# Kernel tuning notes

Measured on AMD Instinct MI355X. Metric: run time of the kernel, lower is better.

## Reference

```python
import jax, jax.numpy as jnp
import numpy as np

B, T, C = 4, 4096, 512
H = 64           # head_size
GRAN = 128       # staircase granularity


def staircase_mask(t, g):
    # tril OR block-diagonal blocks of size g (the staircase fills the upper
    # triangle inside each gxg diagonal block)
    i = jnp.arange(t)
    return (i[:, None] >= i[None, :]) | ((i[:, None] // g) == (i[None, :] // g))


def setup_inputs() -> dict:
    key = jax.random.key(0)
    kx, kk, kq, kv = jax.random.split(key, 4)
    scale = 0.02
    return {
        "x": jax.random.normal(kx, (B, T, C), dtype=jnp.float32),
        "Wk": jax.random.normal(kk, (C, H), dtype=jnp.float32) * scale,
        "Wq": jax.random.normal(kq, (C, H), dtype=jnp.float32) * scale,
        "Wv": jax.random.normal(kv, (C, H), dtype=jnp.float32) * scale,
    }


def reference(x, Wk, Wq, Wv):
    # single head of self-attention with staircase mask (dropout off / eval mode)
    k = x @ Wk          # [B,T,H]
    q = x @ Wq          # [B,T,H]
    v = x @ Wv          # [B,T,H]
    wei = jnp.einsum("bth,bsh->bts", q, k) * (H ** -0.5)   # [B,T,T]
    mask = staircase_mask(T, GRAN)                           # [T,T] bool
    wei = jnp.where(mask, wei, -jnp.inf)
    wei = jax.nn.softmax(wei, axis=-1)
    out = jnp.einsum("bts,bsh->bth", wei, v)                 # [B,T,H]
    return out
```

## Files before the change

kernel.cpp:

```cpp
#include <hip/hip_runtime.h>

typedef unsigned short u16;
typedef unsigned int u32;
typedef unsigned long long u64;
typedef __attribute__((ext_vector_type(8))) short short8;
typedef __attribute__((ext_vector_type(4))) float f32x4;

#define T_ 4096
#define QSCALE 0.18033688f
#define CH 2
#define SBAT 1088
#define PSTRIDE 36

#if __has_builtin(__builtin_amdgcn_exp2f)
#define EXP2F(x) __builtin_amdgcn_exp2f(x)
#else
#define EXP2F(x) exp2f(x)
#endif

__device__ __forceinline__ u16 f2bf(float f) {
    unsigned u = __float_as_uint(f);
    u += 0x7FFFu + ((u >> 16) & 1u);
    return (u16)(u >> 16);
}

__global__ __launch_bounds__(256) void wtrans_kernel(
    const float* __restrict__ Wq, const float* __restrict__ Wk,
    const float* __restrict__ Wv, u16* __restrict__ WTf)
{
    const int tid  = blockIdx.x * 256 + threadIdx.x;
    const int frag = tid >> 6;
    const int lane = tid & 63;
    const int ng   = frag >> 4;
    const int kc   = frag & 15;
    const int m    = ng >> 2;
    const float* W = (m == 0) ? Wq : (m == 1) ? Wk : Wv;
    const int h  = (ng & 3) * 16 + (lane & 15);
    const int c0 = kc * 32 + (lane >> 4) * 8;
    short8 v;
    #pragma unroll
    for (int j = 0; j < 8; ++j)
        v[j] = (short)f2bf(W[(c0 + j) * 64 + h]);
    *(short8*)(WTf + (size_t)frag * 512 + lane * 8) = v;
}

__global__ __launch_bounds__(256) void proj_kernel(
    const float* __restrict__ x, const u16* __restrict__ WTf,
    u16* __restrict__ Qf, u16* __restrict__ Kf, u16* __restrict__ Vf)
{
    __shared__ u16 xs[16 * 520];
    __shared__ u16 img[3072];
    const int t    = threadIdx.x;
    const int lane = t & 63;
    const int w    = t >> 6;
    const int l16  = lane & 15;
    const int quad = lane >> 4;
    const int rowbase = blockIdx.x * 16;
    const int bat  = rowbase >> 12;
    const int tloc = rowbase & 4095;

    #pragma unroll
    for (int it = 0; it < 8; ++it) {
        int f   = t + it * 256;
        int row = f >> 7;
        int c4  = (f & 127) * 4;
        f32x4 a = *(const f32x4*)(x + (size_t)(rowbase + row) * 512 + c4);
        unsigned lo = (unsigned)f2bf(a[0]) | ((unsigned)f2bf(a[1]) << 16);
        unsigned hi = (unsigned)f2bf(a[2]) | ((unsigned)f2bf(a[3]) << 16);
        *(uint2*)(xs + row * 520 + c4) = make_uint2(lo, hi);
    }
    __syncthreads();

    f32x4 acc[3];
    #pragma unroll
    for (int nt = 0; nt < 3; ++nt) acc[nt] = (f32x4){0.f, 0.f, 0.f, 0.f};

    const u16* ab = xs + l16 * 520 + quad * 8;
    const u16* wb = WTf + (size_t)(w * 3 * 16) * 512 + lane * 8;

    #pragma unroll 4
    for (int kc = 0; kc < 16; ++kc) {
        short8 af = *(const short8*)(ab + kc * 32);
        #pragma unroll
        for (int nt = 0; nt < 3; ++nt) {
            short8 bf = *(const short8*)(wb + (size_t)(nt * 16 + kc) * 512);
            acc[nt] = __builtin_amdgcn_mfma_f32_16x16x32_bf16(af, bf, acc[nt], 0, 0, 0);
        }
    }

    #pragma unroll
    for (int nt = 0; nt < 3; ++nt) {
        int ng = w * 3 + nt;
        if (ng < 8) {
            int ng4  = ng & 3;
            float sc = (ng < 4) ? QSCALE : 1.0f;
            u16* ib  = img + ((ng < 4) ? 0 : 1024) + (ng4 >> 1) * 512
                          + ((ng4 & 1) * 2 + (l16 >> 3)) * 128 + (l16 & 7);
            #pragma unroll
            for (int i = 0; i < 4; ++i)
                ib[(quad * 4 + i) * 8] = f2bf(acc[nt][i] * sc);
        } else {
            int nt2  = ng - 8;
            unsigned lo = (unsigned)f2bf(acc[nt][0]) | ((unsigned)f2bf(acc[nt][1]) << 16);
            unsigned hi = (unsigned)f2bf(acc[nt][2]) | ((unsigned)f2bf(acc[nt][3]) << 16);
            *(uint2*)(img + 2048 + nt2 * 256 + (quad >> 1) * 128 + l16 * 8
                          + (quad & 1) * 4) = make_uint2(lo, hi);
        }
    }
    __syncthreads();

    const int tb   = tloc >> 4;
    const int kt   = tloc >> 7;
    const int ks   = (tloc >> 5) & 3;
    const int half = (tloc >> 4) & 1;
    uint2 vq = *(uint2*)(img + t * 4);
    uint2 vk = *(uint2*)(img + 1024 + t * 4);
    uint2 vv = *(uint2*)(img + 2048 + t * 4);
    *(uint2*)(Qf + (size_t)(bat * 256 + tb) * 1024 + t * 4) = vq;
    *(uint2*)(Kf + (size_t)(bat * 256 + tb) * 1024 + t * 4) = vk;
    const int nt2c = t >> 6;
    *(uint2*)(Vf + (size_t)((bat * 32 + kt) * 4 + ks) * 2048
                 + nt2c * 512 + half * 256 + (t & 63) * 4) = vv;
}

__global__ __launch_bounds__(256, 4) void attn_kernel(
    const u16* __restrict__ Qf, const u16* __restrict__ Kf,
    const u16* __restrict__ Vf, u32* __restrict__ pnum,
    float* __restrict__ pden, float* __restrict__ out)
{
    __shared__ u16 Ps[4][2][16 * PSTRIDE];

    const int w    = threadIdx.x >> 6;
    const int lane = threadIdx.x & 63;
    const int l16  = lane & 15;
    const int qd   = lane >> 4;
    const int xcd  = blockIdx.x & 7;
    const int bat  = xcd >> 1;
    const int tw   = ((blockIdx.x >> 3) * 2 + (xcd & 1)) * 4 + w;

    int A = 31, pre = 0, cc = 1;
    for (;;) {
        cc = (A + CH) / CH;
        int cnt4 = 4 * cc;
        if (tw < pre + cnt4) break;
        pre += cnt4; --A;
    }
    const int r    = tw - pre;
    const int c    = r >> 2;
    const int b_   = r & 3;
    const int nkt  = A + 1;
    const int q32  = 4 * A + b_;
    const int kt0  = c * CH;
    const int kt1  = min(kt0 + CH, nkt);
    const int slot = bat * SBAT + pre + b_ + 4 * c;

    short8 aq[2][2];
    #pragma unroll
    for (int g = 0; g < 2; ++g)
        #pragma unroll
        for (int f = 0; f < 2; ++f)
            aq[g][f] = *(const short8*)(Qf
                + ((size_t)((bat * 256 + q32 * 2 + g) * 2 + f)) * 512 + lane * 8);

    short8 ones;
    #pragma unroll
    for (int j = 0; j < 8; ++j) ones[j] = (short)0x3F80;

    f32x4 acc[2][4];
    f32x4 accden[2];
    #pragma unroll
    for (int g = 0; g < 2; ++g) {
        accden[g] = (f32x4){0.f, 0.f, 0.f, 0.f};
        for (int n = 0; n < 4; ++n) acc[g][n] = (f32x4){0.f, 0.f, 0.f, 0.f};
    }

    u16* Pw[2] = { &Ps[w][0][0], &Ps[w][1][0] };

    auto body = [&](int kt) __attribute__((always_inline)) {
        const u16* kfb = Kf + ((size_t)(bat * 256 + kt * 8) * 2) * 512 + lane * 8;
        const u16* vfb = Vf + ((size_t)((bat * 32 + kt) * 16)) * 512 + lane * 8;
        #pragma unroll
        for (int ks = 0; ks < 4; ++ks) {
            #pragma unroll
            for (int b = 0; b < 2; ++b) {
                int nt = 2 * ks + b;
                short8 k0 = *(const short8*)(kfb + (size_t)nt * 1024);
                short8 k1 = *(const short8*)(kfb + (size_t)nt * 1024 + 512);
                #pragma unroll
                for (int g = 0; g < 2; ++g) {
                    f32x4 st = (f32x4){0.f, 0.f, 0.f, 0.f};
                    st = __builtin_amdgcn_mfma_f32_16x16x32_bf16(k0, aq[g][0], st, 0, 0, 0);
                    st = __builtin_amdgcn_mfma_f32_16x16x32_bf16(k1, aq[g][1], st, 0, 0, 0);
                    float p0 = EXP2F(st[0]);
                    float p1 = EXP2F(st[1]);
                    float p2 = EXP2F(st[2]);
                    float p3 = EXP2F(st[3]);
                    u32 q01 = __builtin_amdgcn_perm(__float_as_uint(p1), __float_as_uint(p0), 0x07060302u);
                    u32 q23 = __builtin_amdgcn_perm(__float_as_uint(p3), __float_as_uint(p2), 0x07060302u);
                    u64 pv = (u64)q01 | ((u64)q23 << 32);
                    *(u64*)(Pw[g] + l16 * PSTRIDE + b * 16 + qd * 4) = pv;
                }
            }
            short8 ap[2];
            #pragma unroll
            for (int g = 0; g < 2; ++g)
                ap[g] = *(const short8*)(Pw[g] + l16 * PSTRIDE + qd * 8);
            accden[0] = __builtin_amdgcn_mfma_f32_16x16x32_bf16(ones, ap[0], accden[0], 0, 0, 0);
            accden[1] = __builtin_amdgcn_mfma_f32_16x16x32_bf16(ones, ap[1], accden[1], 0, 0, 0);
            #pragma unroll
            for (int nt2 = 0; nt2 < 4; ++nt2) {
                short8 av = *(const short8*)(vfb + (size_t)(ks * 4 + nt2) * 512);
                acc[0][nt2] = __builtin_amdgcn_mfma_f32_16x16x32_bf16(av, ap[0], acc[0][nt2], 0, 0, 0);
                acc[1][nt2] = __builtin_amdgcn_mfma_f32_16x16x32_bf16(av, ap[1], acc[1][nt2], 0, 0, 0);
            }
        }
    };

    body(kt0);
    if (kt0 + 1 < kt1) body(kt0 + 1);

    float den[2] = { accden[0][0], accden[1][0] };

    if (cc == 1) {
        const float rd0 = 1.0f / den[0];
        const float rd1 = 1.0f / den[1];
        float* op = out + ((size_t)(bat * T_ + q32 * 32 + l16)) * 64 + qd * 4;
        #pragma unroll
        for (int g = 0; g < 2; ++g) {
            const float rd = g ? rd1 : rd0;
            #pragma unroll
            for (int nt2 = 0; nt2 < 4; ++nt2) {
                f32x4 v;
                #pragma unroll
                for (int i = 0; i < 4; ++i) v[i] = acc[g][nt2][i] * rd;
                *(f32x4*)(op + (size_t)g * 16 * 64 + nt2 * 16) = v;
            }
        }
    } else {
        u32* np = pnum + (size_t)slot * 1024;
        #pragma unroll
        for (int g = 0; g < 2; ++g)
            #pragma unroll
            for (int nt2 = 0; nt2 < 4; ++nt2) {
                u32 lo = (u32)f2bf(acc[g][nt2][0]) | ((u32)f2bf(acc[g][nt2][1]) << 16);
                u32 hi = (u32)f2bf(acc[g][nt2][2]) | ((u32)f2bf(acc[g][nt2][3]) << 16);
                u64 val = (u64)lo | ((u64)hi << 32);
                __builtin_nontemporal_store(val, (u64*)(np + (g * 4 + nt2) * 128 + lane * 2));
            }
        if (lane < 32)
            __builtin_nontemporal_store(den[lane >> 4],
                                        &pden[(size_t)slot * 32 + lane]);
    }
}

__global__ __launch_bounds__(256) void fin_kernel(
    const u32* __restrict__ pnum, const float* __restrict__ pden,
    float* __restrict__ out)
{
    __shared__ float sden[8][32];
    __shared__ float rden[32];
    const int blk  = blockIdx.x;
    const int xcd  = blk & 7;
    const int bat  = xcd >> 1;
    const int rest = blk >> 3;
    const int q32  = (rest & 63) * 2 + (xcd & 1);
    const int hh   = rest >> 6;
    const int A = q32 >> 2, b = q32 & 3;
    const int cc = (A + CH) / CH;
    if (cc == 1) return;
    int pre = 0;
    for (int j = 31; j > A; --j) pre += 4 * ((j + CH) / CH);
    const int base = bat * SBAT + pre + b;

    {
        const int md  = threadIdx.x & 31;
        const int grp = threadIdx.x >> 5;
        float d = 0.f;
        for (int ci = grp; ci < cc; ci += 8)
            d += pden[(size_t)(base + 4 * ci) * 32 + md];
        sden[grp][md] = d;
    }
    __syncthreads();
    if (threadIdx.x < 32) {
        float d = 0.f;
        #pragma unroll
        for (int g2 = 0; g2 < 8; ++g2) d += sden[g2][threadIdx.x];
        rden[threadIdx.x] = 1.0f / d;
    }
    __syncthreads();

    const int m   = threadIdx.x >> 3;
    const int g   = m >> 4;
    const int l16 = m & 15;
    const int h0  = hh * 32 + (threadIdx.x & 7) * 4;
    const int nt2 = h0 >> 4;
    const int q0  = (h0 >> 2) & 3;
    const int off = (g * 4 + nt2) * 128 + q0 * 32 + l16 * 2;

    float sv0 = 0.f, sv1 = 0.f, sv2 = 0.f, sv3 = 0.f;
    const u32* sp = pnum + (size_t)base * 1024 + off;
    uint2 cur = *(const uint2*)sp;
    for (int ci = 1; ci < cc; ++ci) {
        uint2 nxt = *(const uint2*)(sp + (size_t)ci * 4096);
        sv0 += __uint_as_float(cur.x << 16);
        sv1 += __uint_as_float(cur.x & 0xFFFF0000u);
        sv2 += __uint_as_float(cur.y << 16);
        sv3 += __uint_as_float(cur.y & 0xFFFF0000u);
        cur = nxt;
    }
    sv0 += __uint_as_float(cur.x << 16);
    sv1 += __uint_as_float(cur.x & 0xFFFF0000u);
    sv2 += __uint_as_float(cur.y << 16);
    sv3 += __uint_as_float(cur.y & 0xFFFF0000u);

    const float rd = rden[m];
    float* op = out + (size_t)(bat * T_ + q32 * 32 + m) * 64 + h0;
    f32x4 r;
    r[0] = sv0 * rd; r[1] = sv1 * rd; r[2] = sv2 * rd; r[3] = sv3 * rd;
    *(f32x4*)op = r;
}

extern "C" void kernel_launch(void* const* d_in, const int* in_sizes, int n_in,
                              void* d_out, int out_size, void* d_ws, size_t ws_size,
                              hipStream_t stream)
{
    const float* x  = (const float*)d_in[0];
    const float* Wk = (const float*)d_in[1];
    const float* Wq = (const float*)d_in[2];
    const float* Wv = (const float*)d_in[3];
    float* out = (float*)d_out;

    u16* ws  = (u16*)d_ws;
    u16* WTf = ws;
    u16* Qf  = ws + 131072;
    u16* Kf  = Qf + 1048576;
    u16* Vf  = Kf + 1048576;
    u32*   pnum = (u32*)(Vf + 1048576);
    float* pden = (float*)(pnum + (size_t)4 * SBAT * 1024);

    wtrans_kernel<<<48, 256, 0, stream>>>(Wq, Wk, Wv, WTf);
    proj_kernel<<<1024, 256, 0, stream>>>(x, WTf, Qf, Kf, Vf);
    attn_kernel<<<SBAT, 256, 0, stream>>>(Qf, Kf, Vf, pnum, pden, out);
    fin_kernel<<<1024, 256, 0, stream>>>(pnum, pden, out);
}
```

Before: 118.0 us.

## Stage shared K/V tiles in LDS cooperatively across the block's waves

```diff
diff --git a/kernel.cpp b/kernel.cpp
--- a/kernel.cpp
+++ b/kernel.cpp
@@ -123,11 +123,12 @@
                  + nt2c * 512 + half * 256 + (t & 63) * 4) = vv;
 }
 
-__global__ __launch_bounds__(256, 4) void attn_kernel(
+__global__ __launch_bounds__(256, 2) void attn_kernel(
     const u16* __restrict__ Qf, const u16* __restrict__ Kf,
     const u16* __restrict__ Vf, u32* __restrict__ pnum,
     float* __restrict__ pden, float* __restrict__ out)
 {
+    __shared__ u16 KVs[32768];
     __shared__ u16 Ps[4][2][16 * PSTRIDE];
 
     const int w    = threadIdx.x >> 6;
@@ -153,6 +154,7 @@
     const int kt0  = c * CH;
     const int kt1  = min(kt0 + CH, nkt);
     const int slot = bat * SBAT + pre + b_ + 4 * c;
+    const int tiles = kt1 - kt0;
 
     short8 aq[2][2];
     #pragma unroll
@@ -162,6 +164,19 @@
             aq[g][f] = *(const short8*)(Qf
                 + ((size_t)((bat * 256 + q32 * 2 + g) * 2 + f)) * 512 + lane * 8);
 
+    {
+        const short8* gk = (const short8*)(Kf + ((size_t)(bat * 256 + kt0 * 8) * 2) * 512);
+        const short8* gv = (const short8*)(Vf + ((size_t)((bat * 32 + kt0) * 16)) * 512);
+        short8* lk = (short8*)&KVs[0];
+        short8* lv = (short8*)&KVs[16384];
+        const int nv = tiles * 1024;
+        for (int o = threadIdx.x; o < nv; o += 256) {
+            lk[o] = gk[o];
+            lv[o] = gv[o];
+        }
+    }
+    __syncthreads();
+
     short8 ones;
     #pragma unroll
     for (int j = 0; j < 8; ++j) ones[j] = (short)0x3F80;
@@ -176,16 +191,16 @@
 
     u16* Pw[2] = { &Ps[w][0][0], &Ps[w][1][0] };
 
-    auto body = [&](int kt) __attribute__((always_inline)) {
-        const u16* kfb = Kf + ((size_t)(bat * 256 + kt * 8) * 2) * 512 + lane * 8;
-        const u16* vfb = Vf + ((size_t)((bat * 32 + kt) * 16)) * 512 + lane * 8;
+    auto body = [&](int tt) __attribute__((always_inline)) {
+        const u16* kfb = KVs + tt * 8192 + lane * 8;
+        const u16* vfb = KVs + 16384 + tt * 8192 + lane * 8;
         #pragma unroll
         for (int ks = 0; ks < 4; ++ks) {
             #pragma unroll
             for (int b = 0; b < 2; ++b) {
                 int nt = 2 * ks + b;
-                short8 k0 = *(const short8*)(kfb + (size_t)nt * 1024);
-                short8 k1 = *(const short8*)(kfb + (size_t)nt * 1024 + 512);
+                short8 k0 = *(const short8*)(kfb + nt * 1024);
+                short8 k1 = *(const short8*)(kfb + nt * 1024 + 512);
                 #pragma unroll
                 for (int g = 0; g < 2; ++g) {
                     f32x4 st = (f32x4){0.f, 0.f, 0.f, 0.f};
@@ -209,15 +224,15 @@
             accden[1] = __builtin_amdgcn_mfma_f32_16x16x32_bf16(ones, ap[1], accden[1], 0, 0, 0);
             #pragma unroll
             for (int nt2 = 0; nt2 < 4; ++nt2) {
-                short8 av = *(const short8*)(vfb + (size_t)(ks * 4 + nt2) * 512);
+                short8 av = *(const short8*)(vfb + (ks * 4 + nt2) * 512);
                 acc[0][nt2] = __builtin_amdgcn_mfma_f32_16x16x32_bf16(av, ap[0], acc[0][nt2], 0, 0, 0);
                 acc[1][nt2] = __builtin_amdgcn_mfma_f32_16x16x32_bf16(av, ap[1], acc[1][nt2], 0, 0, 0);
             }
         }
     };
 
-    body(kt0);
-    if (kt0 + 1 < kt1) body(kt0 + 1);
+    body(0);
+    if (tiles == 2) body(1);
 
     float den[2] = { accden[0][0], accden[1][0] };
 
```

Result: slower. 124.4 us (+5.5%).
